# Optimization experiments

Measured on AMD Instinct MI355X. Metric: run time of the kernel, lower is better.

Reference implementation:

```python
import jax, jax.numpy as jnp
import numpy as np

N_SKILL = 50000
B = 4096          # number of (job, resume) pairs; n_job == n_resume required by the concat
E = 65536         # edges per relation (avg degree 16)
D = 1536          # embedding_dim
HID = [512, 256, 64]


def setup_inputs() -> dict:
    key = jax.random.key(0)
    ks = jax.random.split(key, 16)
    nrm = lambda k, shape, s=0.02: jax.random.normal(k, shape, dtype=jnp.float32) * s
    inp = {
        "x_skill": jax.random.normal(ks[0], (N_SKILL, D), dtype=jnp.float32),
        "x_job": jax.random.normal(ks[1], (B, D), dtype=jnp.float32),
        "x_resume": jax.random.normal(ks[2], (B, D), dtype=jnp.float32),
        "src_sj": jax.random.randint(ks[3], (E,), 0, N_SKILL),
        "dst_sj": jax.random.randint(ks[4], (E,), 0, B),
        "src_sr": jax.random.randint(ks[5], (E,), 0, N_SKILL),
        "dst_sr": jax.random.randint(ks[6], (E,), 0, B),
        "W_rel_j": nrm(ks[7], (D, D)),
        "b_rel_j": jnp.zeros((D,), jnp.float32),
        "W_root_j": nrm(ks[8], (D, D)),
        "W_rel_r": nrm(ks[9], (D, D)),
        "b_rel_r": jnp.zeros((D,), jnp.float32),
        "W_root_r": nrm(ks[10], (D, D)),
        "W1": nrm(ks[11], (2 * D, HID[0])), "b1": jnp.zeros((HID[0],), jnp.float32),
        "W2": nrm(ks[12], (HID[0], HID[1])), "b2": jnp.zeros((HID[1],), jnp.float32),
        "W3": nrm(ks[13], (HID[1], HID[2])), "b3": jnp.zeros((HID[2],), jnp.float32),
        "W4": nrm(ks[14], (HID[2], 1)), "b4": jnp.zeros((1,), jnp.float32),
    }
    return inp


def _graph_conv(x_src, x_dst, src, dst, W_rel, b_rel, W_root):
    # PyG GraphConv (aggr='add', bipartite): out = lin_rel(sum_{j in N(i)} x_j) + lin_root(x_i)
    agg = jax.ops.segment_sum(x_src[src], dst, num_segments=x_dst.shape[0])  # [B, D]
    return agg @ W_rel + b_rel + x_dst @ W_root


def reference(x_skill, x_job, x_resume, src_sj, dst_sj, src_sr, dst_sr,
              W_rel_j, b_rel_j, W_root_j, W_rel_r, b_rel_r, W_root_r,
              W1, b1, W2, b2, W3, b3, W4, b4):
    # HeteroConv: each dst node type ('job', 'resume') receives exactly one relation,
    # so the cross-relation 'mean' aggregation is the identity.
    h_job = jax.nn.relu(_graph_conv(x_skill, x_job, src_sj, dst_sj, W_rel_j, b_rel_j, W_root_j))
    h_res = jax.nn.relu(_graph_conv(x_skill, x_resume, src_sr, dst_sr, W_rel_r, b_rel_r, W_root_r))
    h = jnp.concatenate([h_job, h_res], axis=1)  # [B, 2D]
    # MLP (dropout is inference-mode identity)
    h = jax.nn.relu(h @ W1 + b1)
    h = jax.nn.relu(h @ W2 + b2)
    h = jax.nn.relu(h @ W3 + b3)
    score = (h @ W4 + b4).squeeze(-1)  # [B]
    return score
```

## Files before the change

### kernel.cpp

```cpp
#include <hip/hip_runtime.h>

#define E_EDGES 65536
#define NB 4096
#define DD 1536
#define CAP 96

typedef unsigned short u16;
typedef __bf16 bf16x8 __attribute__((ext_vector_type(8)));
typedef float f32x4 __attribute__((ext_vector_type(4)));

#define AS1(p) ((const __attribute__((address_space(1))) void*)(p))
#define AS3(p) ((__attribute__((address_space(3))) void*)(p))

#define BAR() do { __builtin_amdgcn_s_barrier(); asm volatile("" ::: "memory"); } while (0)
#define VMCNT2() asm volatile("s_waitcnt vmcnt(2)" ::: "memory")
#define VMCNT0() asm volatile("s_waitcnt vmcnt(0)" ::: "memory")

__device__ __forceinline__ u16 f2bf(float f) {
    unsigned u = __float_as_uint(f);
    u += 0x7fffu + ((u >> 16) & 1u);
    return (u16)(u >> 16);
}


__global__ __launch_bounds__(256) void bucket_kernel(
    const int* __restrict__ sj, const int* __restrict__ dj,
    const int* __restrict__ sr, const int* __restrict__ dr,
    int* __restrict__ cnt, int* __restrict__ bkt) {
    int e = blockIdx.x * 256 + threadIdx.x;
    int rel = blockIdx.y;
    int s = rel ? sr[e] : sj[e];
    int d = rel ? dr[e] : dj[e];
    int slot = rel * NB + d;
    int pos = atomicAdd(&cnt[slot], 1);
    if (pos < CAP) bkt[(size_t)slot * CAP + pos] = s;
}


__global__ __launch_bounds__(128) void agg_cvt_kernel(
    const float* __restrict__ xskill, const float* __restrict__ xj, const float* __restrict__ xr,
    const int* __restrict__ bkt, const int* __restrict__ cnt,
    u16* __restrict__ Aj, u16* __restrict__ Ar) {
    int rel = blockIdx.y;
    int row = blockIdx.x;
    int t = threadIdx.x;
    const float* xd = (rel ? xr : xj) + (size_t)row * DD;
    u16* A = (rel ? Ar : Aj) + (size_t)row * (2 * DD);

    float4 v[3];
#pragma unroll
    for (int c = 0; c < 3; ++c) v[c] = *(const float4*)(xd + t * 4 + c * 512);
#pragma unroll
    for (int c = 0; c < 3; ++c) {
        ushort4 o = {f2bf(v[c].x), f2bf(v[c].y), f2bf(v[c].z), f2bf(v[c].w)};
        *(ushort4*)(A + DD + t * 4 + c * 512) = o;
    }

    int count = cnt[rel * NB + row];
    if (count > CAP) count = CAP;
    __shared__ int sidx[CAP];
    if (t < count) sidx[t] = bkt[(size_t)(rel * NB + row) * CAP + t];
    __syncthreads();

    float4 acc[3] = {};
    for (int e = 0; e < count; ++e) {
        const float* xs = xskill + (size_t)sidx[e] * DD;
#pragma unroll
        for (int c = 0; c < 3; ++c) {
            float4 u = *(const float4*)(xs + t * 4 + c * 512);
            acc[c].x += u.x; acc[c].y += u.y; acc[c].z += u.z; acc[c].w += u.w;
        }
    }
#pragma unroll
    for (int c = 0; c < 3; ++c) {
        ushort4 o = {f2bf(acc[c].x), f2bf(acc[c].y), f2bf(acc[c].z), f2bf(acc[c].w)};
        *(ushort4*)(A + t * 4 + c * 512) = o;
    }
}


__global__ __launch_bounds__(256) void transpose_all(
    const float* __restrict__ w0, const float* __restrict__ w1,
    const float* __restrict__ w2, const float* __restrict__ w3,
    const float* __restrict__ w4, const float* __restrict__ w5,
    u16* __restrict__ Wjt, u16* __restrict__ Wrt,
    u16* __restrict__ W1t, u16* __restrict__ W2t) {
    int bid = blockIdx.x;
    const float* in; u16* out; int N, ldo, k0, nbx;
    if (bid < 9216) {
        int m = bid / 2304;
        bid = bid % 2304;
        in = (m == 0) ? w0 : (m == 1) ? w1 : (m == 2) ? w2 : w3;
        out = (m < 2) ? Wjt : Wrt;
        N = 1536; ldo = 3072; k0 = (m & 1) ? DD : 0; nbx = 48;
    } else if (bid < 10752) {
        bid -= 9216;
        in = w4; out = W1t; N = 512; ldo = 3072; k0 = 0; nbx = 16;
    } else {
        bid -= 10752;
        in = w5; out = W2t; N = 256; ldo = 512; k0 = 0; nbx = 8;
    }
    int bx = (bid % nbx) * 32;
    int by = (bid / nbx) * 32;
    __shared__ float tile[32][33];
    int tx = threadIdx.x & 31, ty = threadIdx.x >> 5;
#pragma unroll
    for (int i = 0; i < 4; ++i)
        tile[ty + i * 8][tx] = in[(size_t)(by + ty + i * 8) * N + bx + tx];
    __syncthreads();
#pragma unroll
    for (int i = 0; i < 4; ++i) {
        int n = bx + ty + i * 8;
        int k = by + tx;
        out[(size_t)n * ldo + k0 + k] = f2bf(tile[tx][ty + i * 8]);
    }
}


__global__ __launch_bounds__(512, 2) void conv_gemm256(
    const u16* __restrict__ Aj, const u16* __restrict__ Wjt, const float* __restrict__ bj,
    const u16* __restrict__ Ar, const u16* __restrict__ Wrt, const float* __restrict__ br,
    u16* __restrict__ C) {
    constexpr int K = 3072, NT = K / 64, LDC = 3072;
    __shared__ u16 lds[65536];
    int tid = threadIdx.x;
    int lane = tid & 63;
    int w = tid >> 6;

    int bid = blockIdx.y * 16 + blockIdx.x;
    bid = (bid & 7) * 12 + (bid >> 3);
    long bm = (long)(bid % 16) * 256;
    long bn = (long)(bid / 16) * 256;

    const u16* A; const u16* Bt; const float* bias; long cofs;
    if (blockIdx.z) { A = Ar; Bt = Wrt; bias = br; cofs = DD; }
    else            { A = Aj; Bt = Wjt; bias = bj; cofs = 0;  }

    int wm = (w >> 2) * 128;
    int wn = (w & 3) * 64;

    const int sr0 = (w * 2) * 8 + (lane >> 3);
    const int sr1 = (w * 2 + 1) * 8 + (lane >> 3);
    const int skf = ((lane & 7) * 8) ^ ((lane >> 3) << 3);

    auto stageA = [&](int b, int h, long k0) {
        const u16* g0 = A + (bm + h * 128 + sr0) * (long)K + k0 + skf;
        const u16* g1 = A + (bm + h * 128 + sr1) * (long)K + k0 + skf;
        __builtin_amdgcn_global_load_lds(AS1(g0), AS3(lds + b * 32768 + h * 8192 + (w * 2 + 0) * 512), 16, 0, 0);
        __builtin_amdgcn_global_load_lds(AS1(g1), AS3(lds + b * 32768 + h * 8192 + (w * 2 + 1) * 512), 16, 0, 0);
    };
    auto stageB = [&](int b, int h, long k0) {
        const u16* g0 = Bt + (bn + h * 128 + sr0) * (long)K + k0 + skf;
        const u16* g1 = Bt + (bn + h * 128 + sr1) * (long)K + k0 + skf;
        __builtin_amdgcn_global_load_lds(AS1(g0), AS3(lds + b * 32768 + 16384 + h * 8192 + (w * 2 + 0) * 512), 16, 0, 0);
        __builtin_amdgcn_global_load_lds(AS1(g1), AS3(lds + b * 32768 + 16384 + h * 8192 + (w * 2 + 1) * 512), 16, 0, 0);
    };

    const int lrow = lane & 15;
    const int lko = (lane >> 4) * 8;
    const int rsw = (lane & 7) << 3;

    auto ldA = [&](int b, int mi, int kk) -> bf16x8 {
        return *(const bf16x8*)(lds + b * 32768 + (wm + mi * 16 + lrow) * 64 + ((kk + lko) ^ rsw));
    };
    auto ldB = [&](int b, int nj, int kk) -> bf16x8 {
        return *(const bf16x8*)(lds + b * 32768 + 16384 + (wn + nj * 16 + lrow) * 64 + ((kk + lko) ^ rsw));
    };

    f32x4 acc[8][4] = {};
    bf16x8 bfr[4];

    stageA(0, 0, 0); stageA(0, 1, 0);
    stageB(0, 0, 0); stageB(0, 1, 0);

    for (int t = 0; t < NT; ++t) {
        int b = t & 1;
        long k1 = (long)(t + 1) * 64;
        bool pf = (t + 1 < NT);

        if (pf) { stageA(b ^ 1, 0, k1); VMCNT2(); } else { VMCNT0(); }
        BAR();
        {
            bf16x8 af[4];
#pragma unroll
            for (int mi = 0; mi < 4; ++mi) af[mi] = ldA(b, mi, 0);
#pragma unroll
            for (int nj = 0; nj < 4; ++nj) bfr[nj] = ldB(b, nj, 0);
            __builtin_amdgcn_s_setprio(1);
#pragma unroll
            for (int mi = 0; mi < 4; ++mi)
#pragma unroll
                for (int nj = 0; nj < 4; ++nj)
                    acc[mi][nj] = __builtin_amdgcn_mfma_f32_16x16x32_bf16(af[mi], bfr[nj], acc[mi][nj], 0, 0, 0);
            __builtin_amdgcn_s_setprio(0);
        }
        BAR();
        {
            bf16x8 af[4];
#pragma unroll
            for (int mi = 0; mi < 4; ++mi) af[mi] = ldA(b, 4 + mi, 0);
            if (pf) stageA(b ^ 1, 1, k1);
            BAR();
            __builtin_amdgcn_s_setprio(1);
#pragma unroll
            for (int mi = 0; mi < 4; ++mi)
#pragma unroll
                for (int nj = 0; nj < 4; ++nj)
                    acc[4 + mi][nj] = __builtin_amdgcn_mfma_f32_16x16x32_bf16(af[mi], bfr[nj], acc[4 + mi][nj], 0, 0, 0);
            __builtin_amdgcn_s_setprio(0);
        }
        BAR();
        {
            bf16x8 af[4];
#pragma unroll
            for (int mi = 0; mi < 4; ++mi) af[mi] = ldA(b, mi, 32);
#pragma unroll
            for (int nj = 0; nj < 4; ++nj) bfr[nj] = ldB(b, nj, 32);
            if (pf) stageB(b ^ 1, 0, k1);
            BAR();
            __builtin_amdgcn_s_setprio(1);
#pragma unroll
            for (int mi = 0; mi < 4; ++mi)
#pragma unroll
                for (int nj = 0; nj < 4; ++nj)
                    acc[mi][nj] = __builtin_amdgcn_mfma_f32_16x16x32_bf16(af[mi], bfr[nj], acc[mi][nj], 0, 0, 0);
            __builtin_amdgcn_s_setprio(0);
        }
        BAR();
        {
            bf16x8 af[4];
#pragma unroll
            for (int mi = 0; mi < 4; ++mi) af[mi] = ldA(b, 4 + mi, 32);
            if (pf) stageB(b ^ 1, 1, k1);
            BAR();
            __builtin_amdgcn_s_setprio(1);
#pragma unroll
            for (int mi = 0; mi < 4; ++mi)
#pragma unroll
                for (int nj = 0; nj < 4; ++nj)
                    acc[4 + mi][nj] = __builtin_amdgcn_mfma_f32_16x16x32_bf16(af[mi], bfr[nj], acc[4 + mi][nj], 0, 0, 0);
            __builtin_amdgcn_s_setprio(0);
        }
        BAR();
    }

    int rb = (lane >> 4) * 4, cl = lane & 15;
#pragma unroll
    for (int mi = 0; mi < 8; ++mi)
#pragma unroll
        for (int nj = 0; nj < 4; ++nj) {
            long row = bm + wm + mi * 16 + rb;
            long col = bn + wn + nj * 16 + cl;
            float bb = bias[col];
#pragma unroll
            for (int r = 0; r < 4; ++r) {
                float v = fmaxf(acc[mi][nj][r] + bb, 0.f);
                C[(row + r) * (long)LDC + cofs + col] = f2bf(v);
            }
        }
}


template <int BM, bool OUT_BF16>
__global__ __launch_bounds__(256) void gemm_bias_relu(
    const u16* __restrict__ A, const u16* __restrict__ Bt, const float* __restrict__ bias,
    void* __restrict__ C, int K, int ldc) {
    constexpr int BK = 64;
    constexpr int MI = BM / 32;
    constexpr int NITER = (BM + 128) / 32;
    __shared__ u16 lA[BM * BK];
    __shared__ u16 lB[128 * BK];
    int tid = threadIdx.x;
    int lane = tid & 63;
    int w = tid >> 6;
    long bm = (long)blockIdx.x * BM;
    long bn = (long)blockIdx.y * 128;
    int wm = (w >> 1) * (BM / 2), wn = (w & 1) * 64;
    f32x4 acc[MI][4] = {};
    const int lrow = lane & 15;
    const int lko = (lane >> 4) * 8;

    for (int k0 = 0; k0 < K; k0 += BK) {
#pragma unroll
        for (int i = 0; i < NITER; ++i) {
            int chunk = i * 256 + tid;
            int row = chunk >> 3, kc = chunk & 7;
            if (row < BM) {
                const u16* g = A + (bm + row) * (long)K + k0 + kc * 8;
                __builtin_amdgcn_global_load_lds(AS1(g), AS3((char*)lA + i * 4096 + w * 1024), 16, 0, 0);
            } else {
                const u16* g = Bt + (bn + row - BM) * (long)K + k0 + kc * 8;
                __builtin_amdgcn_global_load_lds(AS1(g), AS3((char*)lB + i * 4096 + w * 1024 - BM * 128), 16, 0, 0);
            }
        }
        __syncthreads();
#pragma unroll
        for (int kk = 0; kk < BK; kk += 32) {
            bf16x8 af[MI], bfr[4];
#pragma unroll
            for (int i = 0; i < MI; ++i)
                af[i] = *(const bf16x8*)(lA + (wm + i * 16 + lrow) * BK + kk + lko);
#pragma unroll
            for (int j = 0; j < 4; ++j)
                bfr[j] = *(const bf16x8*)(lB + (wn + j * 16 + lrow) * BK + kk + lko);
#pragma unroll
            for (int i = 0; i < MI; ++i)
#pragma unroll
                for (int j = 0; j < 4; ++j)
                    acc[i][j] = __builtin_amdgcn_mfma_f32_16x16x32_bf16(af[i], bfr[j], acc[i][j], 0, 0, 0);
        }
        __syncthreads();
    }

    int rb = (lane >> 4) * 4, cl = lane & 15;
#pragma unroll
    for (int i = 0; i < MI; ++i)
#pragma unroll
        for (int j = 0; j < 4; ++j) {
            long row = bm + wm + i * 16 + rb;
            long col = bn + wn + j * 16 + cl;
            float b = bias[col];
#pragma unroll
            for (int r = 0; r < 4; ++r) {
                float v = fmaxf(acc[i][j][r] + b, 0.f);
                long o = (row + r) * (long)ldc + col;
                if (OUT_BF16)
                    ((u16*)C)[o] = f2bf(v);
                else
                    ((float*)C)[o] = v;
            }
        }
}


__global__ __launch_bounds__(64) void l34_kernel(
    const float* __restrict__ h2, const float* __restrict__ W3, const float* __restrict__ b3,
    const float* __restrict__ W4, const float* __restrict__ b4, float* __restrict__ out) {
    int t = threadIdx.x;
    __shared__ float hrow[256];
    float w4t = W4[t];
    float b3t = b3[t];
    for (int rr = 0; rr < 4; ++rr) {
        int row = blockIdx.x * 4 + rr;
        __syncthreads();
        ((float4*)hrow)[t] = ((const float4*)(h2 + (size_t)row * 256))[t];
        __syncthreads();
        float acc = b3t;
#pragma unroll 8
        for (int k = 0; k < 256; ++k) acc = fmaf(hrow[k], W3[k * 64 + t], acc);
        acc = fmaxf(acc, 0.f);
        float s = acc * w4t;
#pragma unroll
        for (int o = 32; o > 0; o >>= 1) s += __shfl_down(s, o);
        if (t == 0) out[row] = s + b4[0];
    }
}


extern "C" void kernel_launch(void* const* d_in, const int* in_sizes, int n_in,
                              void* d_out, int out_size, void* d_ws, size_t ws_size,
                              hipStream_t stream) {
    (void)in_sizes; (void)n_in; (void)out_size; (void)ws_size;
    const float* x_skill  = (const float*)d_in[0];
    const float* x_job    = (const float*)d_in[1];
    const float* x_resume = (const float*)d_in[2];
    const int* src_sj = (const int*)d_in[3];
    const int* dst_sj = (const int*)d_in[4];
    const int* src_sr = (const int*)d_in[5];
    const int* dst_sr = (const int*)d_in[6];
    const float* W_rel_j  = (const float*)d_in[7];
    const float* b_rel_j  = (const float*)d_in[8];
    const float* W_root_j = (const float*)d_in[9];
    const float* W_rel_r  = (const float*)d_in[10];
    const float* b_rel_r  = (const float*)d_in[11];
    const float* W_root_r = (const float*)d_in[12];
    const float* W1 = (const float*)d_in[13];
    const float* b1 = (const float*)d_in[14];
    const float* W2 = (const float*)d_in[15];
    const float* b2 = (const float*)d_in[16];
    const float* W3 = (const float*)d_in[17];
    const float* b3 = (const float*)d_in[18];
    const float* W4 = (const float*)d_in[19];
    const float* b4 = (const float*)d_in[20];
    float* out = (float*)d_out;

    char* p = (char*)d_ws;
    auto alloc = [&](size_t bytes) -> char* {
        char* r = p;
        p += (bytes + 255) & ~(size_t)255;
        return r;
    };
    int* cnt = (int*)alloc(2 * NB * 4);
    int* bkt = (int*)alloc((size_t)2 * NB * CAP * 4);
    u16* Aj   = (u16*)alloc((size_t)NB * 2 * DD * 2);
    u16* Ar   = (u16*)alloc((size_t)NB * 2 * DD * 2);
    u16* Wjt  = (u16*)alloc((size_t)DD * 2 * DD * 2);
    u16* Wrt  = (u16*)alloc((size_t)DD * 2 * DD * 2);
    u16* W1t  = (u16*)alloc((size_t)512 * 3072 * 2);
    u16* W2t  = (u16*)alloc((size_t)256 * 512 * 2);
    u16* hcat = (u16*)alloc((size_t)NB * 3072 * 2);
    u16* h1   = (u16*)alloc((size_t)NB * 512 * 2);
    float* h2 = (float*)alloc((size_t)NB * 256 * 4);

    hipMemsetAsync(cnt, 0, 2 * NB * 4, stream);
    bucket_kernel<<<dim3(E_EDGES / 256, 2), 256, 0, stream>>>(src_sj, dst_sj, src_sr, dst_sr, cnt, bkt);
    transpose_all<<<10880, 256, 0, stream>>>(W_rel_j, W_root_j, W_rel_r, W_root_r, W1, W2,
                                             Wjt, Wrt, W1t, W2t);
    agg_cvt_kernel<<<dim3(NB, 2), 128, 0, stream>>>(x_skill, x_job, x_resume, bkt, cnt, Aj, Ar);

    conv_gemm256<<<dim3(16, 6, 2), 512, 0, stream>>>(Aj, Wjt, b_rel_j, Ar, Wrt, b_rel_r, hcat);
    gemm_bias_relu<64, true><<<dim3(NB / 64, 512 / 128), 256, 0, stream>>>(hcat, W1t, b1, h1, 3072, 512);
    gemm_bias_relu<64, false><<<dim3(NB / 64, 256 / 128), 256, 0, stream>>>(h1, W2t, b2, h2, 512, 256);
    l34_kernel<<<NB / 4, 64, 0, stream>>>(h2, W3, b3, W4, b4, out);
}
```

Before: 363.7 us.

## Simplify conv GEMM pipeline, double-buffer MLP GEMM, batch more rows in l34

The conv GEMM drops its fine-grained interleaved prefetch, which issued staged loads between barriered quarter-steps with vmcnt(2), and instead waits for all loads once per k-tile, issues the whole next tile, then computes, removing several barriers per iteration. The MLP GEMM gains a double-buffered LDS pipeline in place of two syncthreads per tile, plus setprio around its MFMAs and a min-waves launch bound. The l34 kernel handles 16 rows per block instead of 4, reusing W3/b3 loads over more rows. The conv change may lose some load/compute overlap, and doubling LDS in the MLP GEMM may lower occupancy.

```diff
diff --git a/kernel.cpp b/kernel.cpp
--- a/kernel.cpp
+++ b/kernel.cpp
@@ -13,7 +13,6 @@
 #define AS3(p) ((__attribute__((address_space(3))) void*)(p))
 
 #define BAR() do { __builtin_amdgcn_s_barrier(); asm volatile("" ::: "memory"); } while (0)
-#define VMCNT2() asm volatile("s_waitcnt vmcnt(2)" ::: "memory")
 #define VMCNT0() asm volatile("s_waitcnt vmcnt(0)" ::: "memory")
 
 __device__ __forceinline__ u16 f2bf(float f) {
@@ -168,80 +167,38 @@
     };
 
     f32x4 acc[8][4] = {};
-    bf16x8 bfr[4];
 
     stageA(0, 0, 0); stageA(0, 1, 0);
     stageB(0, 0, 0); stageB(0, 1, 0);
 
     for (int t = 0; t < NT; ++t) {
         int b = t & 1;
-        long k1 = (long)(t + 1) * 64;
-        bool pf = (t + 1 < NT);
-
-        if (pf) { stageA(b ^ 1, 0, k1); VMCNT2(); } else { VMCNT0(); }
+        VMCNT0();
         BAR();
-        {
-            bf16x8 af[4];
-#pragma unroll
-            for (int mi = 0; mi < 4; ++mi) af[mi] = ldA(b, mi, 0);
-#pragma unroll
-            for (int nj = 0; nj < 4; ++nj) bfr[nj] = ldB(b, nj, 0);
-            __builtin_amdgcn_s_setprio(1);
-#pragma unroll
-            for (int mi = 0; mi < 4; ++mi)
-#pragma unroll
-                for (int nj = 0; nj < 4; ++nj)
-                    acc[mi][nj] = __builtin_amdgcn_mfma_f32_16x16x32_bf16(af[mi], bfr[nj], acc[mi][nj], 0, 0, 0);
-            __builtin_amdgcn_s_setprio(0);
-        }
-        BAR();
-        {
-            bf16x8 af[4];
-#pragma unroll
-            for (int mi = 0; mi < 4; ++mi) af[mi] = ldA(b, 4 + mi, 0);
-            if (pf) stageA(b ^ 1, 1, k1);
-            BAR();
-            __builtin_amdgcn_s_setprio(1);
-#pragma unroll
-            for (int mi = 0; mi < 4; ++mi)
-#pragma unroll
-                for (int nj = 0; nj < 4; ++nj)
-                    acc[4 + mi][nj] = __builtin_amdgcn_mfma_f32_16x16x32_bf16(af[mi], bfr[nj], acc[4 + mi][nj], 0, 0, 0);
-            __builtin_amdgcn_s_setprio(0);
-        }
-        BAR();
-        {
-            bf16x8 af[4];
-#pragma unroll
-            for (int mi = 0; mi < 4; ++mi) af[mi] = ldA(b, mi, 32);
-#pragma unroll
-            for (int nj = 0; nj < 4; ++nj) bfr[nj] = ldB(b, nj, 32);
-            if (pf) stageB(b ^ 1, 0, k1);
-            BAR();
-            __builtin_amdgcn_s_setprio(1);
-#pragma unroll
-            for (int mi = 0; mi < 4; ++mi)
-#pragma unroll
-                for (int nj = 0; nj < 4; ++nj)
-                    acc[mi][nj] = __builtin_amdgcn_mfma_f32_16x16x32_bf16(af[mi], bfr[nj], acc[mi][nj], 0, 0, 0);
-            __builtin_amdgcn_s_setprio(0);
-        }
-        BAR();
-        {
-            bf16x8 af[4];
-#pragma unroll
-            for (int mi = 0; mi < 4; ++mi) af[mi] = ldA(b, 4 + mi, 32);
-            if (pf) stageB(b ^ 1, 1, k1);
-            BAR();
-            __builtin_amdgcn_s_setprio(1);
-#pragma unroll
-            for (int mi = 0; mi < 4; ++mi)
-#pragma unroll
-                for (int nj = 0; nj < 4; ++nj)
-                    acc[4 + mi][nj] = __builtin_amdgcn_mfma_f32_16x16x32_bf16(af[mi], bfr[nj], acc[4 + mi][nj], 0, 0, 0);
-            __builtin_amdgcn_s_setprio(0);
-        }
-        BAR();
+        if (t + 1 < NT) {
+            long k1 = (long)(t + 1) * 64;
+            stageA(b ^ 1, 0, k1); stageA(b ^ 1, 1, k1);
+            stageB(b ^ 1, 0, k1); stageB(b ^ 1, 1, k1);
+        }
+#pragma unroll
+        for (int kk = 0; kk < 64; kk += 32) {
+            bf16x8 bfr[4];
+#pragma unroll
+            for (int nj = 0; nj < 4; ++nj) bfr[nj] = ldB(b, nj, kk);
+#pragma unroll
+            for (int h = 0; h < 2; ++h) {
+                bf16x8 af[4];
+#pragma unroll
+                for (int mi = 0; mi < 4; ++mi) af[mi] = ldA(b, h * 4 + mi, kk);
+                __builtin_amdgcn_s_setprio(1);
+#pragma unroll
+                for (int mi = 0; mi < 4; ++mi)
+#pragma unroll
+                    for (int nj = 0; nj < 4; ++nj)
+                        acc[h * 4 + mi][nj] = __builtin_amdgcn_mfma_f32_16x16x32_bf16(af[mi], bfr[nj], acc[h * 4 + mi][nj], 0, 0, 0);
+                __builtin_amdgcn_s_setprio(0);
+            }
+        }
     }
 
     int rb = (lane >> 4) * 4, cl = lane & 15;
@@ -262,14 +219,14 @@
 
 
 template <int BM, bool OUT_BF16>
-__global__ __launch_bounds__(256) void gemm_bias_relu(
+__global__ __launch_bounds__(256, 2) void gemm_bias_relu(
     const u16* __restrict__ A, const u16* __restrict__ Bt, const float* __restrict__ bias,
     void* __restrict__ C, int K, int ldc) {
     constexpr int BK = 64;
     constexpr int MI = BM / 32;
     constexpr int NITER = (BM + 128) / 32;
-    __shared__ u16 lA[BM * BK];
-    __shared__ u16 lB[128 * BK];
+    constexpr int TILE = (BM + 128) * BK;
+    __shared__ u16 lds[2 * TILE];
     int tid = threadIdx.x;
     int lane = tid & 63;
     int w = tid >> 6;
@@ -280,20 +237,30 @@
     const int lrow = lane & 15;
     const int lko = (lane >> 4) * 8;
 
-    for (int k0 = 0; k0 < K; k0 += BK) {
+    auto stage = [&](int buf, long k0) {
 #pragma unroll
         for (int i = 0; i < NITER; ++i) {
             int chunk = i * 256 + tid;
             int row = chunk >> 3, kc = chunk & 7;
             if (row < BM) {
                 const u16* g = A + (bm + row) * (long)K + k0 + kc * 8;
-                __builtin_amdgcn_global_load_lds(AS1(g), AS3((char*)lA + i * 4096 + w * 1024), 16, 0, 0);
+                __builtin_amdgcn_global_load_lds(AS1(g), AS3((char*)(lds + (size_t)buf * TILE) + i * 4096 + w * 1024), 16, 0, 0);
             } else {
                 const u16* g = Bt + (bn + row - BM) * (long)K + k0 + kc * 8;
-                __builtin_amdgcn_global_load_lds(AS1(g), AS3((char*)lB + i * 4096 + w * 1024 - BM * 128), 16, 0, 0);
+                __builtin_amdgcn_global_load_lds(AS1(g), AS3((char*)(lds + (size_t)buf * TILE) + i * 4096 + w * 1024), 16, 0, 0);
             }
         }
-        __syncthreads();
+    };
+
+    stage(0, 0);
+    const int nt = K / BK;
+    for (int t = 0; t < nt; ++t) {
+        int b = t & 1;
+        VMCNT0();
+        BAR();
+        if (t + 1 < nt) stage(b ^ 1, (long)(t + 1) * BK);
+        const u16* lA = lds + (size_t)b * TILE;
+        const u16* lB = lA + BM * BK;
 #pragma unroll
         for (int kk = 0; kk < BK; kk += 32) {
             bf16x8 af[MI], bfr[4];
@@ -303,13 +270,14 @@
 #pragma unroll
             for (int j = 0; j < 4; ++j)
                 bfr[j] = *(const bf16x8*)(lB + (wn + j * 16 + lrow) * BK + kk + lko);
+            __builtin_amdgcn_s_setprio(1);
 #pragma unroll
             for (int i = 0; i < MI; ++i)
 #pragma unroll
                 for (int j = 0; j < 4; ++j)
                     acc[i][j] = __builtin_amdgcn_mfma_f32_16x16x32_bf16(af[i], bfr[j], acc[i][j], 0, 0, 0);
-        }
-        __syncthreads();
+            __builtin_amdgcn_s_setprio(0);
+        }
     }
 
     int rb = (lane >> 4) * 4, cl = lane & 15;
@@ -340,8 +308,8 @@
     __shared__ float hrow[256];
     float w4t = W4[t];
     float b3t = b3[t];
-    for (int rr = 0; rr < 4; ++rr) {
-        int row = blockIdx.x * 4 + rr;
+    for (int rr = 0; rr < 16; ++rr) {
+        int row = blockIdx.x * 16 + rr;
         __syncthreads();
         ((float4*)hrow)[t] = ((const float4*)(h2 + (size_t)row * 256))[t];
         __syncthreads();
@@ -411,5 +379,5 @@
     conv_gemm256<<<dim3(16, 6, 2), 512, 0, stream>>>(Aj, Wjt, b_rel_j, Ar, Wrt, b_rel_r, hcat);
     gemm_bias_relu<64, true><<<dim3(NB / 64, 512 / 128), 256, 0, stream>>>(hcat, W1t, b1, h1, 3072, 512);
     gemm_bias_relu<64, false><<<dim3(NB / 64, 256 / 128), 256, 0, stream>>>(h1, W2t, b2, h2, 512, 256);
-    l34_kernel<<<NB / 4, 64, 0, stream>>>(h2, W3, b3, W4, b4, out);
-}
+    l34_kernel<<<NB / 16, 64, 0, stream>>>(h2, W3, b3, W4, b4, out);
+}
```

Result: slower. 380.7 us, median of 2 (+4.7%).
